# Optimization experiments

Measured on AMD Instinct MI355X. Metric: run time of the kernel, lower is better.

The kernel has to match this reference:

```python
import jax, jax.numpy as jnp
import numpy as np


def setup_inputs() -> dict:
    key = jax.random.key(0)
    kY, kH = jax.random.split(key)
    B, M, L, S = 4, 512, 31, 2
    W = M + L - 1  # 542: dispersed measurement width
    Y = jax.random.uniform(kY, (B, M, W, S), dtype=jnp.float32)
    H = jax.random.uniform(kH, (B, M, M, L), dtype=jnp.float32)
    return {"Y": Y, "H": H}


def reference(Y, H):
    # Y: [B, M, W, S] measurement (W = M+L-1), H: [B, M, M, L] coded aperture
    B, M, W, S = Y.shape
    L = H.shape[-1]
    # tf.roll(Y, -i, axis=2)[:, :, 0:M] == Y[:, :, (j+i) % W] for j in [0, M)
    idx = (jnp.arange(M)[:, None] + jnp.arange(L)[None, :]) % W  # [M, L]
    Xs = Y[:, :, idx, :]                      # [B, M, M, L, S] shifted volume
    X = jnp.sum(H[..., None] * Xs, axis=4)    # sum over shots -> [B, M, M, L]
    return X / jnp.max(X)
```

## Files before the change

### kernel.cpp

```cpp
#include <hip/hip_runtime.h>

#define CB 4
#define CM 512
#define CL 31
#define CW 542
#define SLAB  (CM * CL)
#define SLAB4 (SLAB / 4)
#define NBM   (CB * CM)
#define CPAD  543

typedef float f32x4 __attribute__((ext_vector_type(4)));


__device__ __forceinline__ void stage_ysum(const float* __restrict__ Y, int bm,
                                           float* __restrict__ ys) {
    const float2* y2 = (const float2*)(Y + (size_t)bm * (CW * 2));
    for (int j = threadIdx.x; j < CW; j += 256) {
        float2 v = y2[j];
        float s = v.x + v.y;
        ys[j]            = s;
        ys[j + CPAD]     = s;
        ys[j + 2 * CPAD] = s;
        ys[j + 3 * CPAD] = s;
    }
}

struct IdxState {
    int l0;
    int i0;
};

__device__ __forceinline__ IdxState idx_init(int tid) {
    unsigned f = 4u * (unsigned)tid;
    unsigned n = f / 31u;
    IdxState s;
    s.l0 = (int)(f - n * 31u);
    s.i0 = (int)n + s.l0;
    return s;
}

__device__ __forceinline__ void idx_quad(const IdxState& s,
                                         int& i0, int& i1, int& i2, int& i3) {
    i0 = s.i0;
    i1 = s.i0 + ((s.l0 >= 30) ? 1 - 30 : 1);
    i2 = s.i0 + ((s.l0 >= 29) ? 2 - 30 : 2);
    i3 = s.i0 + ((s.l0 >= 28) ? 3 - 30 : 3);
}

__device__ __forceinline__ void idx_step(IdxState& s) {
    bool w = (s.l0 == 30);
    s.i0 += w ? 4 : 34;
    s.l0  = w ? 0 : (s.l0 + 1);
}

__device__ __forceinline__ float quad_max(const f32x4& h, const float* __restrict__ ys,
                                          const IdxState& st) {
    int i0, i1, i2, i3;
    idx_quad(st, i0, i1, i2, i3);
    return fmaxf(fmaxf(h[0] * ys[i0], h[1] * ys[i1]),
                 fmaxf(h[2] * ys[i2], h[3] * ys[i3]));
}

__global__ __launch_bounds__(256, 8) void cassi_max_k(
    const float* __restrict__ Y,
    const float* __restrict__ H,
    float* __restrict__ blockmax)
{
    __shared__ float ysum[4 * CPAD];
    __shared__ float smax[4];
    const int bm  = blockIdx.x;
    const int tid = threadIdx.x;

    const f32x4* h4 = (const f32x4*)(H + (size_t)bm * SLAB);
    f32x4 h0 = h4[tid];
    f32x4 h1 = h4[tid + 256];

    stage_ysum(Y, bm, ysum);
    __syncthreads();

    const float* ys = ysum + ((tid >> 3) & 3) * CPAD;
    IdxState st = idx_init(tid);
    float mx = 0.0f;

    mx = fmaxf(mx, quad_max(h0, ys, st)); idx_step(st);
    mx = fmaxf(mx, quad_max(h1, ys, st)); idx_step(st);

#pragma unroll 5
    for (int k = 2; k < 15; ++k) {
        f32x4 h = h4[tid + (k << 8)];
        mx = fmaxf(mx, quad_max(h, ys, st));
        idx_step(st);
    }
    if (tid < 128) {
        f32x4 h = h4[tid + 15 * 256];
        mx = fmaxf(mx, quad_max(h, ys, st));
    }

#pragma unroll
    for (int off = 32; off > 0; off >>= 1)
        mx = fmaxf(mx, __shfl_down(mx, off, 64));
    if ((tid & 63) == 0) smax[tid >> 6] = mx;
    __syncthreads();
    if (tid == 0)
        blockmax[bm] = fmaxf(fmaxf(smax[0], smax[1]), fmaxf(smax[2], smax[3]));
}

__global__ __launch_bounds__(256, 8) void cassi_out_k(
    const float* __restrict__ Y,
    const float* __restrict__ H,
    const float* __restrict__ blockmax,
    float* __restrict__ out)
{
    __shared__ float ysum[4 * CPAD];
    __shared__ float smax[4];
    const int bm  = blockIdx.x;
    const int tid = threadIdx.x;

    const f32x4* h4 = (const f32x4*)(H + (size_t)bm * SLAB);
    f32x4 h0 = h4[tid];
    f32x4 h1 = h4[tid + 256];

    stage_ysum(Y, bm, ysum);

    float m = 0.0f;
    for (int j = tid; j < NBM; j += 256) m = fmaxf(m, blockmax[j]);
#pragma unroll
    for (int off = 32; off > 0; off >>= 1)
        m = fmaxf(m, __shfl_down(m, off, 64));
    if ((tid & 63) == 0) smax[tid >> 6] = m;
    __syncthreads();
    const float inv = 1.0f / fmaxf(fmaxf(smax[0], smax[1]), fmaxf(smax[2], smax[3]));

    const float* ys = ysum + ((tid >> 3) & 3) * CPAD;
    f32x4* o4 = (f32x4*)(out + (size_t)bm * SLAB);
    IdxState st = idx_init(tid);

    {
        int i0, i1, i2, i3;
        idx_quad(st, i0, i1, i2, i3);
        f32x4 o = { h0[0] * ys[i0] * inv, h0[1] * ys[i1] * inv,
                    h0[2] * ys[i2] * inv, h0[3] * ys[i3] * inv };
        __builtin_nontemporal_store(o, &o4[tid]);
        idx_step(st);
    }
    {
        int i0, i1, i2, i3;
        idx_quad(st, i0, i1, i2, i3);
        f32x4 o = { h1[0] * ys[i0] * inv, h1[1] * ys[i1] * inv,
                    h1[2] * ys[i2] * inv, h1[3] * ys[i3] * inv };
        __builtin_nontemporal_store(o, &o4[tid + 256]);
        idx_step(st);
    }

#pragma unroll 5
    for (int k = 2; k < 15; ++k) {
        f32x4 h = h4[tid + (k << 8)];
        int i0, i1, i2, i3;
        idx_quad(st, i0, i1, i2, i3);
        f32x4 o = { h[0] * ys[i0] * inv, h[1] * ys[i1] * inv,
                    h[2] * ys[i2] * inv, h[3] * ys[i3] * inv };
        __builtin_nontemporal_store(o, &o4[tid + (k << 8)]);
        idx_step(st);
    }
    if (tid < 128) {
        f32x4 h = h4[tid + 15 * 256];
        int i0, i1, i2, i3;
        idx_quad(st, i0, i1, i2, i3);
        f32x4 o = { h[0] * ys[i0] * inv, h[1] * ys[i1] * inv,
                    h[2] * ys[i2] * inv, h[3] * ys[i3] * inv };
        __builtin_nontemporal_store(o, &o4[tid + 15 * 256]);
    }
}

extern "C" void kernel_launch(void* const* d_in, const int* in_sizes, int n_in,
                              void* d_out, int out_size, void* d_ws, size_t ws_size,
                              hipStream_t stream)
{
    (void)in_sizes; (void)n_in; (void)out_size; (void)ws_size;
    const float* Y = (const float*)d_in[0];
    const float* H = (const float*)d_in[1];
    float* out = (float*)d_out;
    float* blockmax = (float*)d_ws;

    cassi_max_k<<<NBM, 256, 0, stream>>>(Y, H, blockmax);
    cassi_out_k<<<NBM, 256, 0, stream>>>(Y, H, blockmax, out);
}
```

Before: 252.7 us.

## Write unnormalized product in first pass, then rescale output in place

The first kernel now writes the unnormalized H*sum(Y) product to the output while computing block maxima. The second kernel only reads back that output and multiplies by the inverse global max, so it no longer re-reads H, restages Y, or recomputes the gather. This trades a second read of H for a read-modify-write of the output, and drops the nontemporal stores, hoping the output stays in cache.

```diff
diff --git a/kernel.cpp b/kernel.cpp
--- a/kernel.cpp
+++ b/kernel.cpp
@@ -53,18 +53,23 @@
     s.l0  = w ? 0 : (s.l0 + 1);
 }
 
-__device__ __forceinline__ float quad_max(const f32x4& h, const float* __restrict__ ys,
-                                          const IdxState& st) {
+__device__ __forceinline__ f32x4 quad_x(const f32x4& h, const float* __restrict__ ys,
+                                        const IdxState& st) {
     int i0, i1, i2, i3;
     idx_quad(st, i0, i1, i2, i3);
-    return fmaxf(fmaxf(h[0] * ys[i0], h[1] * ys[i1]),
-                 fmaxf(h[2] * ys[i2], h[3] * ys[i3]));
+    f32x4 x = { h[0] * ys[i0], h[1] * ys[i1], h[2] * ys[i2], h[3] * ys[i3] };
+    return x;
 }
 
-__global__ __launch_bounds__(256, 8) void cassi_max_k(
+__device__ __forceinline__ float quad_fold(const f32x4& x) {
+    return fmaxf(fmaxf(x[0], x[1]), fmaxf(x[2], x[3]));
+}
+
+__global__ __launch_bounds__(256, 8) void cassi_xmax(
     const float* __restrict__ Y,
     const float* __restrict__ H,
-    float* __restrict__ blockmax)
+    float* __restrict__ blockmax,
+    float* __restrict__ out)
 {
     __shared__ float ysum[4 * CPAD];
     __shared__ float smax[4];
@@ -79,21 +84,36 @@
     __syncthreads();
 
     const float* ys = ysum + ((tid >> 3) & 3) * CPAD;
+    f32x4* o4 = (f32x4*)(out + (size_t)bm * SLAB);
     IdxState st = idx_init(tid);
     float mx = 0.0f;
 
-    mx = fmaxf(mx, quad_max(h0, ys, st)); idx_step(st);
-    mx = fmaxf(mx, quad_max(h1, ys, st)); idx_step(st);
+    {
+        f32x4 x = quad_x(h0, ys, st);
+        o4[tid] = x;
+        mx = fmaxf(mx, quad_fold(x));
+        idx_step(st);
+    }
+    {
+        f32x4 x = quad_x(h1, ys, st);
+        o4[tid + 256] = x;
+        mx = fmaxf(mx, quad_fold(x));
+        idx_step(st);
+    }
 
-#pragma unroll 5
+#pragma unroll 4
     for (int k = 2; k < 15; ++k) {
         f32x4 h = h4[tid + (k << 8)];
-        mx = fmaxf(mx, quad_max(h, ys, st));
+        f32x4 x = quad_x(h, ys, st);
+        o4[tid + (k << 8)] = x;
+        mx = fmaxf(mx, quad_fold(x));
         idx_step(st);
     }
     if (tid < 128) {
         f32x4 h = h4[tid + 15 * 256];
-        mx = fmaxf(mx, quad_max(h, ys, st));
+        f32x4 x = quad_x(h, ys, st);
+        o4[tid + 15 * 256] = x;
+        mx = fmaxf(mx, quad_fold(x));
     }
 
 #pragma unroll
@@ -105,25 +125,19 @@
         blockmax[bm] = fmaxf(fmaxf(smax[0], smax[1]), fmaxf(smax[2], smax[3]));
 }
 
-__global__ __launch_bounds__(256, 8) void cassi_out_k(
-    const float* __restrict__ Y,
-    const float* __restrict__ H,
+__global__ __launch_bounds__(256, 8) void cassi_scale(
     const float* __restrict__ blockmax,
     float* __restrict__ out)
 {
-    __shared__ float ysum[4 * CPAD];
     __shared__ float smax[4];
     const int bm  = blockIdx.x;
     const int tid = threadIdx.x;
 
-    const f32x4* h4 = (const f32x4*)(H + (size_t)bm * SLAB);
-    f32x4 h0 = h4[tid];
-    f32x4 h1 = h4[tid + 256];
-
-    stage_ysum(Y, bm, ysum);
-
-    float m = 0.0f;
-    for (int j = tid; j < NBM; j += 256) m = fmaxf(m, blockmax[j]);
+    const f32x4* b4 = (const f32x4*)blockmax;
+    f32x4 a = b4[tid];
+    f32x4 b = b4[tid + 256];
+    float m = fmaxf(fmaxf(fmaxf(a[0], a[1]), fmaxf(a[2], a[3])),
+                    fmaxf(fmaxf(b[0], b[1]), fmaxf(b[2], b[3])));
 #pragma unroll
     for (int off = 32; off > 0; off >>= 1)
         m = fmaxf(m, __shfl_down(m, off, 64));
@@ -131,44 +145,17 @@
     __syncthreads();
     const float inv = 1.0f / fmaxf(fmaxf(smax[0], smax[1]), fmaxf(smax[2], smax[3]));
 
-    const float* ys = ysum + ((tid >> 3) & 3) * CPAD;
     f32x4* o4 = (f32x4*)(out + (size_t)bm * SLAB);
-    IdxState st = idx_init(tid);
-
-    {
-        int i0, i1, i2, i3;
-        idx_quad(st, i0, i1, i2, i3);
-        f32x4 o = { h0[0] * ys[i0] * inv, h0[1] * ys[i1] * inv,
-                    h0[2] * ys[i2] * inv, h0[3] * ys[i3] * inv };
-        __builtin_nontemporal_store(o, &o4[tid]);
-        idx_step(st);
-    }
-    {
-        int i0, i1, i2, i3;
-        idx_quad(st, i0, i1, i2, i3);
-        f32x4 o = { h1[0] * ys[i0] * inv, h1[1] * ys[i1] * inv,
-                    h1[2] * ys[i2] * inv, h1[3] * ys[i3] * inv };
-        __builtin_nontemporal_store(o, &o4[tid + 256]);
-        idx_step(st);
-    }
-
 #pragma unroll 5
-    for (int k = 2; k < 15; ++k) {
-        f32x4 h = h4[tid + (k << 8)];
-        int i0, i1, i2, i3;
-        idx_quad(st, i0, i1, i2, i3);
-        f32x4 o = { h[0] * ys[i0] * inv, h[1] * ys[i1] * inv,
-                    h[2] * ys[i2] * inv, h[3] * ys[i3] * inv };
-        __builtin_nontemporal_store(o, &o4[tid + (k << 8)]);
-        idx_step(st);
+    for (int k = 0; k < 15; ++k) {
+        f32x4 v = o4[tid + (k << 8)];
+        v[0] *= inv; v[1] *= inv; v[2] *= inv; v[3] *= inv;
+        o4[tid + (k << 8)] = v;
     }
     if (tid < 128) {
-        f32x4 h = h4[tid + 15 * 256];
-        int i0, i1, i2, i3;
-        idx_quad(st, i0, i1, i2, i3);
-        f32x4 o = { h[0] * ys[i0] * inv, h[1] * ys[i1] * inv,
-                    h[2] * ys[i2] * inv, h[3] * ys[i3] * inv };
-        __builtin_nontemporal_store(o, &o4[tid + 15 * 256]);
+        f32x4 v = o4[tid + 15 * 256];
+        v[0] *= inv; v[1] *= inv; v[2] *= inv; v[3] *= inv;
+        o4[tid + 15 * 256] = v;
     }
 }
 
@@ -182,6 +169,6 @@
     float* out = (float*)d_out;
     float* blockmax = (float*)d_ws;
 
-    cassi_max_k<<<NBM, 256, 0, stream>>>(Y, H, blockmax);
-    cassi_out_k<<<NBM, 256, 0, stream>>>(Y, H, blockmax, out);
+    cassi_xmax<<<NBM, 256, 0, stream>>>(Y, H, blockmax, out);
+    cassi_scale<<<NBM, 256, 0, stream>>>(blockmax, out);
 }
```

After: 273.7 us. 8.3% more time.
